# Kernel optimization log

Hardware: AMD Instinct MI355X
Metric: run time of the kernel (lower is better)

## Reference

```python
import jax, jax.numpy as jnp
import numpy as np

EMBED_DIM = 1024
NUM_HEADS = 16
HEAD_DIM = EMBED_DIM // NUM_HEADS


def setup_inputs() -> dict:
    key = jax.random.key(0)
    k_x, k_wqkv, k_bqkv, k_wout, k_bout = jax.random.split(key, 5)
    s = 1.0 / np.sqrt(EMBED_DIM)
    return {
        "x": jax.random.normal(k_x, (2, 2048, EMBED_DIM), dtype=jnp.float32),
        "w_qkv": jax.random.uniform(k_wqkv, (EMBED_DIM, 3 * EMBED_DIM), jnp.float32, -s, s),
        "b_qkv": jax.random.uniform(k_bqkv, (3 * EMBED_DIM,), jnp.float32, -s, s),
        "w_out": jax.random.uniform(k_wout, (EMBED_DIM, EMBED_DIM), jnp.float32, -s, s),
        "b_out": jax.random.uniform(k_bout, (EMBED_DIM,), jnp.float32, -s, s),
    }


def reference(x, w_qkv, b_qkv, w_out, b_out):
    B, S, D = x.shape
    H, Hd = NUM_HEADS, HEAD_DIM
    # qkv projection, then per-head chunk: layout matches torch view(B,S,H,3*Hd).chunk(3,-1)
    qkv = (x @ w_qkv + b_qkv).reshape(B, S, H, 3, Hd)  # [B,S,H,3,Hd]
    q = qkv[..., 0, :]  # [B,S,H,Hd]
    k = qkv[..., 1, :]
    v = qkv[..., 2, :]
    scale = 1.0 / np.sqrt(Hd).astype(np.float32)
    scores = jnp.einsum("bqhd,bkhd->bhqk", q, k) * scale  # [B,H,S,S]
    probs = jax.nn.softmax(scores, axis=-1)
    out = jnp.einsum("bhqk,bkhd->bqhd", probs, v).reshape(B, S, D)
    return out @ w_out + b_out
```

## Files before the change

kernel.cpp:

```cpp
#include <hip/hip_runtime.h>
#include <hip/hip_bf16.h>


typedef __bf16 bf16;
typedef __bf16 bf16x8 __attribute__((ext_vector_type(8)));
typedef float  f32x4  __attribute__((ext_vector_type(4)));
typedef float  f32x16 __attribute__((ext_vector_type(16)));
typedef unsigned int uint;
typedef unsigned int uint2v __attribute__((ext_vector_type(2)));

__device__ __forceinline__ void gload_lds16(const void* g, void* l) {
  __builtin_amdgcn_global_load_lds(
      (const __attribute__((address_space(1))) unsigned int*)g,
      (__attribute__((address_space(3))) unsigned int*)l, 16, 0, 0);
}

__device__ __forceinline__ uint pkbf16(float lo, float hi) {
  union { bf16 h[2]; uint u; } t;
  t.h[0] = (bf16)lo; t.h[1] = (bf16)hi;
  return t.u;
}

__device__ __forceinline__ void pl32swapu(uint& a, uint& b) {
  uint2v r = __builtin_amdgcn_permlane32_swap(a, b, false, false);
  a = r.x; b = r.y;
}
__device__ __forceinline__ void pl32swapf(float& a, float& b) {
  uint ua = __builtin_bit_cast(uint, a), ub = __builtin_bit_cast(uint, b);
  pl32swapu(ua, ub);
  a = __builtin_bit_cast(float, ua); b = __builtin_bit_cast(float, ub);
}

__global__ __launch_bounds__(256) void k_convert(const float* __restrict__ in,
                                                 bf16* __restrict__ out, int n) {
  int i = (blockIdx.x * blockDim.x + threadIdx.x) * 8;
  if (i >= n) return;
  float4 a = *(const float4*)(in + i);
  float4 b = *(const float4*)(in + i + 4);
  bf16x8 o;
  o[0] = (bf16)a.x; o[1] = (bf16)a.y; o[2] = (bf16)a.z; o[3] = (bf16)a.w;
  o[4] = (bf16)b.x; o[5] = (bf16)b.y; o[6] = (bf16)b.z; o[7] = (bf16)b.w;
  *(bf16x8*)(out + i) = o;
}

template<bool PERM>
__global__ __launch_bounds__(256) void k_transpose(const float* __restrict__ in,
                                                   bf16* __restrict__ out, int K, int N) {
  __shared__ float tile[32][33];
  int n0 = blockIdx.x * 32, k0 = blockIdx.y * 32;
  int tx = threadIdx.x, ty = threadIdx.y;
#pragma unroll
  for (int i = 0; i < 4; i++)
    tile[ty + i * 8][tx] = in[(size_t)(k0 + ty + i * 8) * N + n0 + tx];
  __syncthreads();
#pragma unroll
  for (int i = 0; i < 4; i++) {
    int n = n0 + ty + i * 8;
    int row = n;
    if (PERM) {
      int rem = n % 192;
      row = (rem >> 6) * 1024 + (n / 192) * 64 + (rem & 63);
    }
    out[(size_t)row * K + k0 + tx] = (bf16)tile[tx][ty + i * 8];
  }
}

template<int BM, int BN>
__device__ __forceinline__ void gemm_tile(const bf16* __restrict__ A, const bf16* __restrict__ B,
                                          int K, int m0, int n0,
                                          bf16* As, bf16* Bs, f32x4 acc[BM / 32][BN / 32]) {
  const int tid  = threadIdx.x;
  const int lane = tid & 63;
  const int wr   = (tid >> 7) & 1;
  const int wc   = (tid >> 6) & 1;
  constexpr int LA = BM / 64, LB = BN / 64;
  auto stage = [&](int k0, int b) {
#pragma unroll
    for (int i = 0; i < LA; i++) {
      int row = i * 64 + (tid >> 2);
      int sw  = (tid & 3) ^ (row & 3);
      gload_lds16(A + (size_t)(m0 + row) * K + k0 + sw * 8, (char*)As + b * (BM * 64) + i * 4096 + tid * 16);
    }
#pragma unroll
    for (int i = 0; i < LB; i++) {
      int row = i * 64 + (tid >> 2);
      int sw  = (tid & 3) ^ (row & 3);
      gload_lds16(B + (size_t)(n0 + row) * K + k0 + sw * 8, (char*)Bs + b * (BN * 64) + i * 4096 + tid * 16);
    }
  };
  const int nk = K / 32;
  stage(0, 0); stage(32, 1); stage(64, 2);
  for (int t = 0; t < nk; t++) {
    if (t < nk - 2) {
      if constexpr (LA + LB == 4) asm volatile("s_waitcnt vmcnt(8)" ::: "memory");
      else                        asm volatile("s_waitcnt vmcnt(6)" ::: "memory");
    } else if (t < nk - 1) {
      if constexpr (LA + LB == 4) asm volatile("s_waitcnt vmcnt(4)" ::: "memory");
      else                        asm volatile("s_waitcnt vmcnt(3)" ::: "memory");
    } else {
      asm volatile("s_waitcnt vmcnt(0)" ::: "memory");
    }
    __builtin_amdgcn_s_barrier();
    asm volatile("" ::: "memory");
    if (t + 3 < nk) stage((t + 3) * 32, (t + 3) & 3);
    const int cur = t & 3;
    bf16x8 af[BM / 32], bfr[BN / 32];
#pragma unroll
    for (int r = 0; r < BM / 32; r++) {
      int ra = wr * (BM / 2) + r * 16 + (lane & 15);
      af[r]  = *(const bf16x8*)((const char*)As + cur * (BM * 64) + ra * 64 + ((((lane >> 4) << 4)) ^ ((ra & 3) << 4)));
    }
#pragma unroll
    for (int c = 0; c < BN / 32; c++) {
      int rb = wc * (BN / 2) + c * 16 + (lane & 15);
      bfr[c] = *(const bf16x8*)((const char*)Bs + cur * (BN * 64) + rb * 64 + ((((lane >> 4) << 4)) ^ ((rb & 3) << 4)));
    }
#pragma unroll
    for (int r = 0; r < BM / 32; r++)
#pragma unroll
      for (int c = 0; c < BN / 32; c++)
        acc[r][c] = __builtin_amdgcn_mfma_f32_16x16x32_bf16(af[r], bfr[c], acc[r][c], 0, 0, 0);
    asm volatile("" ::: "memory");
  }
}

__global__ __launch_bounds__(512, 2) void k_gemm_qkv(const bf16* __restrict__ A, const bf16* __restrict__ Bt,
                                                     const float* __restrict__ bias,
                                                     bf16* __restrict__ qb, bf16* __restrict__ kb,
                                                     bf16* __restrict__ vtb) {
  __shared__ char GS[131072];
  const int tid  = threadIdx.x;
  const int lane = tid & 63;
  const int wave = tid >> 6;
  const int wr   = wave >> 2;
  const int wc   = wave & 3;
  const int m0 = blockIdx.x * 256, n0 = blockIdx.y * 256;
  const int K = 1024;

  f32x4 acc[8][4];
  f32x4 zero = {0.f, 0.f, 0.f, 0.f};
#pragma unroll
  for (int ms = 0; ms < 8; ms++)
#pragma unroll
    for (int ns = 0; ns < 4; ns++) acc[ms][ns] = zero;

  auto stage = [&](int t, int b) {
    int k0 = t * 64;
#pragma unroll
    for (int i = 0; i < 4; i++) {
      int cid = i * 512 + tid;
      int row = cid >> 3, c = cid & 7;
      gload_lds16(A + (size_t)(m0 + row) * K + k0 + ((c ^ (row & 7)) * 8),
                  GS + b * 32768 + cid * 16);
    }
#pragma unroll
    for (int i = 0; i < 4; i++) {
      int cid = i * 512 + tid;
      int row = cid >> 3, c = cid & 7;
      gload_lds16(Bt + (size_t)(n0 + row) * K + k0 + ((c ^ (row & 7)) * 8),
                  GS + 65536 + b * 32768 + cid * 16);
    }
  };

  stage(0, 0);
  for (int t = 0; t < 16; t++) {
    const int b = t & 1;
    if (t + 1 < 16) {
      stage(t + 1, b ^ 1);
      asm volatile("s_waitcnt vmcnt(8)" ::: "memory");
    } else {
      asm volatile("s_waitcnt vmcnt(0)" ::: "memory");
    }
    __builtin_amdgcn_s_barrier();
    asm volatile("" ::: "memory");
    const char* Ab = GS + b * 32768;
    const char* Bb = GS + 65536 + b * 32768;
#pragma unroll
    for (int ks = 0; ks < 2; ks++) {
      bf16x8 af[8], bf_[4];
#pragma unroll
      for (int ms = 0; ms < 8; ms++) {
        int row = wr * 128 + ms * 16 + (lane & 15);
        int ch = (ks * 4 + (lane >> 4)) ^ (row & 7);
        af[ms] = *(const bf16x8*)(Ab + row * 128 + ch * 16);
      }
#pragma unroll
      for (int ns = 0; ns < 4; ns++) {
        int row = wc * 64 + ns * 16 + (lane & 15);
        int ch = (ks * 4 + (lane >> 4)) ^ (row & 7);
        bf_[ns] = *(const bf16x8*)(Bb + row * 128 + ch * 16);
      }
      __builtin_amdgcn_s_setprio(1);
#pragma unroll
      for (int ms = 0; ms < 8; ms++)
#pragma unroll
        for (int ns = 0; ns < 4; ns++)
          acc[ms][ns] = __builtin_amdgcn_mfma_f32_16x16x32_bf16(af[ms], bf_[ns], acc[ms][ns], 0, 0, 0);
      __builtin_amdgcn_s_setprio(0);
    }
    asm volatile("" ::: "memory");
    __builtin_amdgcn_s_barrier();
    asm volatile("" ::: "memory");
  }

  const int group = n0 >> 10;
  const int hb = (n0 & 1023) >> 6;
  const int b_ = m0 >> 11;
  const float QSs = 0.125f * 1.4426950408889634f;
  char* TL = GS;

  if (group < 2) {
#pragma unroll
    for (int ms = 0; ms < 8; ms++) {
      int mloc = wr * 128 + ms * 16 + ((lane >> 4) << 2);
#pragma unroll
      for (int ns = 0; ns < 4; ns++) {
        int nloc = wc * 64 + ns * 16 + (lane & 15);
        int np = n0 + nloc;
        float bv = bias[((np & 1023) >> 6) * 192 + group * 64 + (np & 63)];
#pragma unroll
        for (int g = 0; g < 4; g++) {
          float v = acc[ms][ns][g] + bv;
          if (group == 0) v *= QSs;
          int m = mloc + g;
          int byte = m * 512 + ((((nloc >> 3) ^ (m & 7)) << 4) | ((nloc & 7) << 1));
          *(bf16*)(TL + byte) = (bf16)v;
        }
      }
    }
    __syncthreads();
    bf16* dst = (group == 0) ? qb : kb;
#pragma unroll
    for (int it = 0; it < 16; it++) {
      int cid = it * 512 + tid;
      int row = cid >> 5, cc = cid & 31;
      int hh = hb + (cc >> 3), ck = cc & 7;
      bf16x8 v8 = *(const bf16x8*)(TL + row * 512 + ((cc ^ (row & 7)) << 4));
      *(bf16x8*)(dst + ((size_t)(b_ * 16 + hh) * 2048 + (m0 & 2047) + row) * 64 + ck * 8) = v8;
    }
  } else {
#pragma unroll
    for (int ms = 0; ms < 8; ms++) {
      int mloc = wr * 128 + ms * 16 + ((lane >> 4) << 2);
#pragma unroll
      for (int ns = 0; ns < 4; ns++) {
        int nloc = wc * 64 + ns * 16 + (lane & 15);
        int np = n0 + nloc;
        float bv = bias[((np & 1023) >> 6) * 192 + 2 * 64 + (np & 63)];
#pragma unroll
        for (int g = 0; g < 4; g++) {
          float v = acc[ms][ns][g] + bv;
          int m = mloc + g;
          int byte = nloc * 512 + ((((m >> 3) ^ (nloc & 7)) << 4) | ((m & 7) << 1));
          *(bf16*)(TL + byte) = (bf16)v;
        }
      }
    }
    __syncthreads();
#pragma unroll
    for (int it = 0; it < 16; it++) {
      int cid = it * 512 + tid;
      int row = cid >> 5, mc = cid & 31;
      int hh = hb + (row >> 6), dd = row & 63;
      bf16x8 v8 = *(const bf16x8*)(TL + row * 512 + ((mc ^ (row & 7)) << 4));
      *(bf16x8*)(vtb + ((size_t)(b_ * 16 + hh) * 64 + dd) * 2048 + (m0 & 2047) + mc * 8) = v8;
    }
  }
}

__global__ __launch_bounds__(256) void k_gemm_out(const bf16* __restrict__ A, const bf16* __restrict__ Bt,
                                                  const float* __restrict__ bias,
                                                  float* __restrict__ out) {
  __shared__ bf16 As[4 * 64 * 32];
  __shared__ bf16 Bs[4 * 128 * 32];
  int m0 = blockIdx.x * 64, n0 = blockIdx.y * 128;
  f32x4 zero = {0.f, 0.f, 0.f, 0.f};
  f32x4 acc[2][4];
#pragma unroll
  for (int r = 0; r < 2; r++)
#pragma unroll
    for (int c = 0; c < 4; c++) acc[r][c] = zero;
  gemm_tile<64, 128>(A, Bt, 1024, m0, n0, As, Bs, acc);
  const int lane = threadIdx.x & 63;
  const int wr = (threadIdx.x >> 7) & 1, wc = (threadIdx.x >> 6) & 1;
#pragma unroll
  for (int r = 0; r < 2; r++) {
    int mbase = m0 + wr * 32 + r * 16 + ((lane >> 4) << 2);
#pragma unroll
    for (int c = 0; c < 4; c++) {
      int n = n0 + wc * 64 + c * 16 + (lane & 15);
      float bv = bias[n];
#pragma unroll
      for (int g = 0; g < 4; g++)
        out[(size_t)(mbase + g) * 1024 + n] = acc[r][c][g] + bv;
    }
  }
}

__global__ __launch_bounds__(512, 4) void k_attn(const bf16* __restrict__ qb, const bf16* __restrict__ kb,
                                                 const bf16* __restrict__ vtb, bf16* __restrict__ ob) {
  __shared__ char SMEM[73728];
  const int tid  = threadIdx.x;
  const int lane = tid & 63;
  const int wave = tid >> 6;
  const int qsub = wave & 3;
  const int half = wave >> 2;
  const int ln31 = lane & 31;
  const int g    = lane >> 5;

  int l = blockIdx.x;
  int x = l & 7, j = l >> 3;
  int qt = j & 15;
  int bh = x * 4 + (j >> 4);

  const int q0 = qt * 128 + qsub * 32;

  bf16x8 qf[4];
  {
    const bf16* qp = qb + ((size_t)bh * 2048 + q0 + ln31) * 64 + g * 8;
#pragma unroll
    for (int dc = 0; dc < 4; dc++) qf[dc] = *(const bf16x8*)(qp + dc * 16);
  }

  const f32x16 z16 = 0.f;
  f32x16 O0 = 0.f, O1 = 0.f;
  float lacc[4] = {0.f, 0.f, 0.f, 0.f};

  const int rbo = ln31 * 144 + (g << 4);
  const char* kbs0 = SMEM + half * 9216 + rbo;
  const char* kbs1 = SMEM + 36864 + half * 9216 + rbo;
  const char* vbs0 = SMEM + 18432 + half * 9216 + rbo;
  const char* vbs1 = SMEM + 36864 + 18432 + half * 9216 + rbo;

  const int c1 = tid, r1 = c1 / 9, cc1 = c1 % 9;
  const int of1 = (cc1 == 8 ? 0 : cc1) * 8;
  const bf16* kg0a = kb  + ((size_t)bh * 2048 +        r1) * 64 + of1;
  const bf16* kg1a = kb  + ((size_t)bh * 2048 + 1024 + r1) * 64 + of1;
  const bf16* vg0a = vtb + ((size_t)bh * 64 + r1) * 2048 +        of1;
  const bf16* vg1a = vtb + ((size_t)bh * 64 + r1) * 2048 + 1024 + of1;
  const int se = tid >> 6;
  const int ce = 512 + (tid & 63), re = ce / 9, cce = ce % 9;
  const int ofe = (cce == 8 ? 0 : cce) * 8;
  const bf16* gext =
      (se == 0) ? kb  + ((size_t)bh * 2048 +        re) * 64 + ofe :
      (se == 1) ? kb  + ((size_t)bh * 2048 + 1024 + re) * 64 + ofe :
      (se == 2) ? vtb + ((size_t)bh * 64 + re) * 2048 +        ofe :
                  vtb + ((size_t)bh * 64 + re) * 2048 + 1024 + ofe;
  const size_t gadv = (se < 2) ? 4096 : 64;
  const int eoff = se * 9216 + ce * 16;

  auto stage = [&](int t, int s) {
    char* bs = SMEM + s * 36864;
    gload_lds16(kg0a + (size_t)t * 4096, bs +         c1 * 16);
    gload_lds16(kg1a + (size_t)t * 4096, bs + 9216  + c1 * 16);
    gload_lds16(vg0a + t * 64,           bs + 18432 + c1 * 16);
    gload_lds16(vg1a + t * 64,           bs + 27648 + c1 * 16);
    if (tid < 256) gload_lds16(gext + (size_t)t * gadv, bs + eoff);
  };

  auto smx = [&](f32x16& sv, bf16x8& f0, bf16x8& f1) {
#pragma unroll
    for (int r = 0; r < 16; r++) sv[r] = __builtin_amdgcn_exp2f(sv[r]);
#pragma unroll
    for (int r = 0; r < 4; r++)
      lacc[r] += (sv[r] + sv[r + 4]) + (sv[r + 8] + sv[r + 12]);
    uint a0 = pkbf16(sv[0], sv[1]), a1 = pkbf16(sv[2], sv[3]);
    uint a2 = pkbf16(sv[4], sv[5]), a3 = pkbf16(sv[6], sv[7]);
    pl32swapu(a0, a2); pl32swapu(a1, a3);
    union { uint w[4]; bf16x8 v; } pa;
    pa.w[0] = a0; pa.w[1] = a1; pa.w[2] = a2; pa.w[3] = a3;
    f0 = pa.v;
    uint b0 = pkbf16(sv[8], sv[9]),  b1 = pkbf16(sv[10], sv[11]);
    uint b2 = pkbf16(sv[12], sv[13]), b3 = pkbf16(sv[14], sv[15]);
    pl32swapu(b0, b2); pl32swapu(b1, b3);
    union { uint w[4]; bf16x8 v; } pb;
    pb.w[0] = b0; pb.w[1] = b1; pb.w[2] = b2; pb.w[3] = b3;
    f1 = pb.v;
  };

  stage(0, 0);
  for (int t = 0; t < 16; t++) {
    asm volatile("s_waitcnt vmcnt(0)" ::: "memory");
    __builtin_amdgcn_s_barrier();
    asm volatile("" ::: "memory");
    if (t + 1 < 16) stage(t + 1, (t + 1) & 1);

    const char* Kb = (t & 1) ? kbs1 : kbs0;
    const char* Vb = (t & 1) ? vbs1 : vbs0;

    f32x16 sA, sB;
    __builtin_amdgcn_s_setprio(1);
    sA = __builtin_amdgcn_mfma_f32_32x32x16_bf16(*(const bf16x8*)(Kb +    0), qf[0], z16, 0, 0, 0);
    sB = __builtin_amdgcn_mfma_f32_32x32x16_bf16(*(const bf16x8*)(Kb + 4608), qf[0], z16, 0, 0, 0);
#pragma unroll
    for (int dc = 1; dc < 4; dc++) {
      sA = __builtin_amdgcn_mfma_f32_32x32x16_bf16(*(const bf16x8*)(Kb + dc * 32),        qf[dc], sA, 0, 0, 0);
      sB = __builtin_amdgcn_mfma_f32_32x32x16_bf16(*(const bf16x8*)(Kb + 4608 + dc * 32), qf[dc], sB, 0, 0, 0);
    }
    __builtin_amdgcn_s_setprio(0);

    bf16x8 fA0, fA1, fB0, fB1;
    smx(sA, fA0, fA1);
    __builtin_amdgcn_s_setprio(1);
    O0 = __builtin_amdgcn_mfma_f32_32x32x16_bf16(*(const bf16x8*)(Vb +    0), fA0, O0, 0, 0, 0);
    O1 = __builtin_amdgcn_mfma_f32_32x32x16_bf16(*(const bf16x8*)(Vb + 4608), fA0, O1, 0, 0, 0);
    O0 = __builtin_amdgcn_mfma_f32_32x32x16_bf16(*(const bf16x8*)(Vb +   32), fA1, O0, 0, 0, 0);
    O1 = __builtin_amdgcn_mfma_f32_32x32x16_bf16(*(const bf16x8*)(Vb + 4640), fA1, O1, 0, 0, 0);
    __builtin_amdgcn_s_setprio(0);
    smx(sB, fB0, fB1);
    __builtin_amdgcn_s_setprio(1);
    O0 = __builtin_amdgcn_mfma_f32_32x32x16_bf16(*(const bf16x8*)(Vb +   64), fB0, O0, 0, 0, 0);
    O1 = __builtin_amdgcn_mfma_f32_32x32x16_bf16(*(const bf16x8*)(Vb + 4672), fB0, O1, 0, 0, 0);
    O0 = __builtin_amdgcn_mfma_f32_32x32x16_bf16(*(const bf16x8*)(Vb +   96), fB1, O0, 0, 0, 0);
    O1 = __builtin_amdgcn_mfma_f32_32x32x16_bf16(*(const bf16x8*)(Vb + 4704), fB1, O1, 0, 0, 0);
    __builtin_amdgcn_s_setprio(0);
    asm volatile("" ::: "memory");
  }

  float l_r = (lacc[0] + lacc[1]) + (lacc[2] + lacc[3]);
  { float o = l_r; pl32swapf(l_r, o); l_r += o; }

  float* Opart = (float*)SMEM;
  float* Ls    = (float*)(SMEM + 36864);
  __syncthreads();
  if (half == 1) {
    float* my = Opart + (qsub * 64 + lane) * 36;
#pragma unroll
    for (int c = 0; c < 4; c++) {
      f32x4 a = {O0[c * 4], O0[c * 4 + 1], O0[c * 4 + 2], O0[c * 4 + 3]};
      f32x4 b = {O1[c * 4], O1[c * 4 + 1], O1[c * 4 + 2], O1[c * 4 + 3]};
      *(f32x4*)(my + c * 4) = a;
      *(f32x4*)(my + 16 + c * 4) = b;
    }
    if (lane < 32) Ls[qsub * 32 + ln31] = l_r;
  }
  __syncthreads();
  bf16 (*Os)[32][72] = reinterpret_cast<bf16 (*)[32][72]>(SMEM + 40960);
  if (half == 0) {
    const float* pr = Opart + (qsub * 64 + lane) * 36;
#pragma unroll
    for (int c = 0; c < 4; c++) {
      f32x4 a = *(const f32x4*)(pr + c * 4);
      f32x4 b = *(const f32x4*)(pr + 16 + c * 4);
#pragma unroll
      for (int k = 0; k < 4; k++) { O0[c * 4 + k] += a[k]; O1[c * 4 + k] += b[k]; }
    }
    l_r += Ls[qsub * 32 + ln31];
    float inv = 1.0f / l_r;
#pragma unroll
    for (int r = 0; r < 16; r++) {
      int d0 = (r & 3) + 8 * (r >> 2) + 4 * g;
      Os[qsub][ln31][d0]      = (bf16)(O0[r] * inv);
      Os[qsub][ln31][d0 + 32] = (bf16)(O1[r] * inv);
    }
  }
  __syncthreads();
  if (half == 0) {
    int b_ = bh >> 4, h = bh & 15;
#pragma unroll
    for (int it = 0; it < 4; it++) {
      int cid = it * 64 + lane;
      int row = cid >> 3, c = cid & 7;
      bf16x8 v8o = *(const bf16x8*)&Os[qsub][row][c * 8];
      *(bf16x8*)(ob + ((size_t)(b_ * 2048 + q0 + row)) * 1024 + h * 64 + c * 8) = v8o;
    }
  }
}

extern "C" void kernel_launch(void* const* d_in, const int* in_sizes, int n_in,
                              void* d_out, int out_size, void* d_ws, size_t ws_size,
                              hipStream_t stream) {
  const float* x     = (const float*)d_in[0];
  const float* w_qkv = (const float*)d_in[1];
  const float* b_qkv = (const float*)d_in[2];
  const float* w_out = (const float*)d_in[3];
  const float* b_out = (const float*)d_in[4];
  float* out = (float*)d_out;

  char* ws = (char*)d_ws;
  bf16* xb  = (bf16*)ws;
  bf16* wqT = (bf16*)(ws + (8ull  << 20));
  bf16* woT = (bf16*)(ws + (14ull << 20));
  bf16* qb  = (bf16*)(ws + (16ull << 20));
  bf16* kb  = (bf16*)(ws + (24ull << 20));
  bf16* vtb = (bf16*)(ws + (32ull << 20));

  k_convert<<<2048, 256, 0, stream>>>(x, xb, 4194304);
  k_transpose<true><<<dim3(96, 32), dim3(32, 8), 0, stream>>>(w_qkv, wqT, 1024, 3072);
  k_transpose<false><<<dim3(32, 32), dim3(32, 8), 0, stream>>>(w_out, woT, 1024, 1024);
  k_gemm_qkv<<<dim3(16, 12), 512, 0, stream>>>(xb, wqT, b_qkv, qb, kb, vtb);
  k_attn<<<512, 512, 0, stream>>>(qb, kb, vtb, xb);
  k_gemm_out<<<dim3(64, 8), 256, 0, stream>>>(xb, woT, b_out, out);
}
```

Before: 116.6 us.

## Software-pipeline attention loop: split K/V staging and overlap QK with PV

Splits tile staging into separate K and V loads and restructures the main loop so that the PV product for tile t runs while the QK product and softmax for tile t+1 are computed, with two tiles of prefetch in flight. The goal is to hide global-to-LDS load latency and the softmax VALU work behind MFMA work by staggering stages across iterations. It adds an extra barrier per iteration and relies on correct double-buffer reuse timing, which carries a risk of races if the wait and barrier placement is wrong.

Result: no change. 116.3 us (-0.2%).

```diff
diff --git a/kernel.cpp b/kernel.cpp
--- a/kernel.cpp
+++ b/kernel.cpp
@@ -349,14 +349,20 @@
   const size_t gadv = (se < 2) ? 4096 : 64;
   const int eoff = se * 9216 + ce * 16;
 
-  auto stage = [&](int t, int s) {
+  auto stageK = [&](int t, int s) {
     char* bs = SMEM + s * 36864;
-    gload_lds16(kg0a + (size_t)t * 4096, bs +         c1 * 16);
-    gload_lds16(kg1a + (size_t)t * 4096, bs + 9216  + c1 * 16);
-    gload_lds16(vg0a + t * 64,           bs + 18432 + c1 * 16);
-    gload_lds16(vg1a + t * 64,           bs + 27648 + c1 * 16);
-    if (tid < 256) gload_lds16(gext + (size_t)t * gadv, bs + eoff);
-  };
+    gload_lds16(kg0a + (size_t)t * 4096, bs +        c1 * 16);
+    gload_lds16(kg1a + (size_t)t * 4096, bs + 9216 + c1 * 16);
+    if (tid < 256 && se < 2) gload_lds16(gext + (size_t)t * gadv, bs + eoff);
+  };
+  auto stageV = [&](int t, int s) {
+    char* bs = SMEM + s * 36864;
+    gload_lds16(vg0a + t * 64, bs + 18432 + c1 * 16);
+    gload_lds16(vg1a + t * 64, bs + 27648 + c1 * 16);
+    if (tid < 256 && se >= 2) gload_lds16(gext + (size_t)t * gadv, bs + eoff);
+  };
+
+  bf16x8 fA0, fA1, fB0, fB1;
 
   auto smx = [&](f32x16& sv, bf16x8& f0, bf16x8& f1) {
 #pragma unroll
@@ -378,18 +384,7 @@
     f1 = pb.v;
   };
 
-  stage(0, 0);
-  for (int t = 0; t < 16; t++) {
-    asm volatile("s_waitcnt vmcnt(0)" ::: "memory");
-    __builtin_amdgcn_s_barrier();
-    asm volatile("" ::: "memory");
-    if (t + 1 < 16) stage(t + 1, (t + 1) & 1);
-
-    const char* Kb = (t & 1) ? kbs1 : kbs0;
-    const char* Vb = (t & 1) ? vbs1 : vbs0;
-
-    f32x16 sA, sB;
-    __builtin_amdgcn_s_setprio(1);
+  auto qk = [&](const char* Kb, f32x16& sA, f32x16& sB) {
     sA = __builtin_amdgcn_mfma_f32_32x32x16_bf16(*(const bf16x8*)(Kb +    0), qf[0], z16, 0, 0, 0);
     sB = __builtin_amdgcn_mfma_f32_32x32x16_bf16(*(const bf16x8*)(Kb + 4608), qf[0], z16, 0, 0, 0);
 #pragma unroll
@@ -397,25 +392,58 @@
       sA = __builtin_amdgcn_mfma_f32_32x32x16_bf16(*(const bf16x8*)(Kb + dc * 32),        qf[dc], sA, 0, 0, 0);
       sB = __builtin_amdgcn_mfma_f32_32x32x16_bf16(*(const bf16x8*)(Kb + 4608 + dc * 32), qf[dc], sB, 0, 0, 0);
     }
-    __builtin_amdgcn_s_setprio(0);
-
-    bf16x8 fA0, fA1, fB0, fB1;
-    smx(sA, fA0, fA1);
-    __builtin_amdgcn_s_setprio(1);
+  };
+
+  auto pv = [&](const char* Vb) {
     O0 = __builtin_amdgcn_mfma_f32_32x32x16_bf16(*(const bf16x8*)(Vb +    0), fA0, O0, 0, 0, 0);
     O1 = __builtin_amdgcn_mfma_f32_32x32x16_bf16(*(const bf16x8*)(Vb + 4608), fA0, O1, 0, 0, 0);
     O0 = __builtin_amdgcn_mfma_f32_32x32x16_bf16(*(const bf16x8*)(Vb +   32), fA1, O0, 0, 0, 0);
     O1 = __builtin_amdgcn_mfma_f32_32x32x16_bf16(*(const bf16x8*)(Vb + 4640), fA1, O1, 0, 0, 0);
-    __builtin_amdgcn_s_setprio(0);
-    smx(sB, fB0, fB1);
-    __builtin_amdgcn_s_setprio(1);
     O0 = __builtin_amdgcn_mfma_f32_32x32x16_bf16(*(const bf16x8*)(Vb +   64), fB0, O0, 0, 0, 0);
     O1 = __builtin_amdgcn_mfma_f32_32x32x16_bf16(*(const bf16x8*)(Vb + 4672), fB0, O1, 0, 0, 0);
     O0 = __builtin_amdgcn_mfma_f32_32x32x16_bf16(*(const bf16x8*)(Vb +   96), fB1, O0, 0, 0, 0);
     O1 = __builtin_amdgcn_mfma_f32_32x32x16_bf16(*(const bf16x8*)(Vb + 4704), fB1, O1, 0, 0, 0);
+  };
+
+  stageK(0, 0); stageV(0, 0);
+  stageK(1, 1); stageV(1, 1);
+  asm volatile("s_waitcnt vmcnt(0)" ::: "memory");
+  __builtin_amdgcn_s_barrier();
+  asm volatile("" ::: "memory");
+  {
+    f32x16 sA, sB;
+    __builtin_amdgcn_s_setprio(1);
+    qk(kbs0, sA, sB);
     __builtin_amdgcn_s_setprio(0);
-    asm volatile("" ::: "memory");
-  }
+    smx(sA, fA0, fA1);
+    smx(sB, fB0, fB1);
+  }
+
+  for (int t = 0; t < 15; t++) {
+    asm volatile("" ::: "memory");
+    __builtin_amdgcn_s_barrier();
+    asm volatile("" ::: "memory");
+    if (t + 2 < 16) stageK(t + 2, t & 1);
+    const char* Vb = (t & 1) ? vbs1 : vbs0;
+    __builtin_amdgcn_s_setprio(1);
+    pv(Vb);
+    __builtin_amdgcn_s_setprio(0);
+    asm volatile("" ::: "memory");
+    __builtin_amdgcn_s_barrier();
+    asm volatile("" ::: "memory");
+    if (t + 2 < 16) stageV(t + 2, t & 1);
+    const char* Kb = (t & 1) ? kbs0 : kbs1;
+    f32x16 sA, sB;
+    __builtin_amdgcn_s_setprio(1);
+    qk(Kb, sA, sB);
+    __builtin_amdgcn_s_setprio(0);
+    smx(sA, fA0, fA1);
+    smx(sB, fB0, fB1);
+    asm volatile("s_waitcnt vmcnt(0)" ::: "memory");
+  }
+  __builtin_amdgcn_s_barrier();
+  asm volatile("" ::: "memory");
+  pv(vbs1);
 
   float l_r = (lacc[0] + lacc[1]) + (lacc[2] + lacc[3]);
   { float o = l_r; pl32swapf(l_r, o); l_r += o; }
```

## Interleave QKV GEMM loads and MFMA in quarter-tile phases with finer barriers

Applied to the files above, without the earlier changes.

Rewrites the main loop of the QKV projection GEMM into a ping-pong schedule. Each K-tile is split into four sub-tile phases (A/B halves), and each phase's LDS reads, global-to-LDS prefetch and MFMA block are separated by barriers so memory traffic overlaps with compute at a finer grain. Global and LDS addresses are precomputed per thread to reduce address arithmetic. The cost is more barriers and a fragile vmcnt accounting that must match the issue order exactly.

After: 112.4 us. -3.6%, faster.

```diff
diff --git a/kernel.cpp b/kernel.cpp
--- a/kernel.cpp
+++ b/kernel.cpp
@@ -74,18 +74,18 @@
   const int wr   = (tid >> 7) & 1;
   const int wc   = (tid >> 6) & 1;
   constexpr int LA = BM / 64, LB = BN / 64;
-  auto stage = [&](int k0, int b) {
+  auto stage = [&](int k0v, int b) {
 #pragma unroll
     for (int i = 0; i < LA; i++) {
       int row = i * 64 + (tid >> 2);
       int sw  = (tid & 3) ^ (row & 3);
-      gload_lds16(A + (size_t)(m0 + row) * K + k0 + sw * 8, (char*)As + b * (BM * 64) + i * 4096 + tid * 16);
+      gload_lds16(A + (size_t)(m0 + row) * K + k0v + sw * 8, (char*)As + b * (BM * 64) + i * 4096 + tid * 16);
     }
 #pragma unroll
     for (int i = 0; i < LB; i++) {
       int row = i * 64 + (tid >> 2);
       int sw  = (tid & 3) ^ (row & 3);
-      gload_lds16(B + (size_t)(n0 + row) * K + k0 + sw * 8, (char*)Bs + b * (BN * 64) + i * 4096 + tid * 16);
+      gload_lds16(B + (size_t)(n0 + row) * K + k0v + sw * 8, (char*)Bs + b * (BN * 64) + i * 4096 + tid * 16);
     }
   };
   const int nk = K / 32;
@@ -144,64 +144,141 @@
 #pragma unroll
     for (int ns = 0; ns < 4; ns++) acc[ms][ns] = zero;
 
-  auto stage = [&](int t, int b) {
-    int k0 = t * 64;
-#pragma unroll
-    for (int i = 0; i < 4; i++) {
-      int cid = i * 512 + tid;
-      int row = cid >> 3, c = cid & 7;
-      gload_lds16(A + (size_t)(m0 + row) * K + k0 + ((c ^ (row & 7)) * 8),
-                  GS + b * 32768 + cid * 16);
-    }
-#pragma unroll
-    for (int i = 0; i < 4; i++) {
-      int cid = i * 512 + tid;
-      int row = cid >> 3, c = cid & 7;
-      gload_lds16(Bt + (size_t)(n0 + row) * K + k0 + ((c ^ (row & 7)) * 8),
-                  GS + 65536 + b * 32768 + cid * 16);
-    }
-  };
-
-  stage(0, 0);
-  for (int t = 0; t < 16; t++) {
-    const int b = t & 1;
-    if (t + 1 < 16) {
-      stage(t + 1, b ^ 1);
-      asm volatile("s_waitcnt vmcnt(8)" ::: "memory");
+  const int ccs = tid & 7;
+  int rA[2], rB[2];
+  {
+    int lr0 = tid >> 3;
+    rA[0] = lr0;
+    rB[0] = (lr0 & 31) + ((lr0 >> 5) << 6);
+    int lr1 = 64 + lr0;
+    rA[1] = (lr1 & 63) + 128;
+    rB[1] = (lr1 & 31) + ((lr1 >> 5) << 6);
+  }
+  const bf16* Agp[2]; const bf16* Bgp[2];
+  int Alo[2], Blo[2];
+#pragma unroll
+  for (int j = 0; j < 2; j++) {
+    Agp[j] = A  + (size_t)(m0 + rA[j]) * K + (ccs ^ (rA[j] & 7)) * 8;
+    Alo[j] = rA[j] * 128 + ccs * 16;
+    Bgp[j] = Bt + (size_t)(n0 + rB[j]) * K + (ccs ^ (rB[j] & 7)) * 8;
+    Blo[j] = rB[j] * 128 + ccs * 16;
+  }
+  auto stA = [&](int t, int h) {
+    int b = t & 1;
+#pragma unroll
+    for (int j = 0; j < 2; j++)
+      gload_lds16(Agp[j] + (size_t)(h * 64) * K + t * 64, GS + b * 32768 + Alo[j] + h * 8192);
+  };
+  auto stB = [&](int t, int h) {
+    int b = t & 1;
+#pragma unroll
+    for (int j = 0; j < 2; j++)
+      gload_lds16(Bgp[j] + (size_t)(h * 32) * K + t * 64, GS + 65536 + b * 32768 + Blo[j] + h * 4096);
+  };
+
+  bf16x8 af[4][2], bf0[2][2], bf1[2][2];
+  auto rdA = [&](const char* Ab, int mh) {
+#pragma unroll
+    for (int ms = 0; ms < 4; ms++)
+#pragma unroll
+      for (int ks = 0; ks < 2; ks++) {
+        int row = wr * 128 + (mh * 4 + ms) * 16 + (lane & 15);
+        int ch = (ks * 4 + (lane >> 4)) ^ (row & 7);
+        af[ms][ks] = *(const bf16x8*)(Ab + row * 128 + ch * 16);
+      }
+  };
+  auto rdB = [&](const char* Bb, int nh, bf16x8 (&bfx)[2][2]) {
+#pragma unroll
+    for (int ns = 0; ns < 2; ns++)
+#pragma unroll
+      for (int ks = 0; ks < 2; ks++) {
+        int row = wc * 64 + (nh * 2 + ns) * 16 + (lane & 15);
+        int ch = (ks * 4 + (lane >> 4)) ^ (row & 7);
+        bfx[ns][ks] = *(const bf16x8*)(Bb + row * 128 + ch * 16);
+      }
+  };
+  auto mm = [&](int mh, int nh, bf16x8 (&bfx)[2][2]) {
+    __builtin_amdgcn_s_setprio(1);
+#pragma unroll
+    for (int ks = 0; ks < 2; ks++)
+#pragma unroll
+      for (int ms = 0; ms < 4; ms++)
+#pragma unroll
+        for (int ns = 0; ns < 2; ns++)
+          acc[mh * 4 + ms][nh * 2 + ns] =
+              __builtin_amdgcn_mfma_f32_16x16x32_bf16(af[ms][ks], bfx[ns][ks],
+                                                      acc[mh * 4 + ms][nh * 2 + ns], 0, 0, 0);
+    __builtin_amdgcn_s_setprio(0);
+  };
+
+#define BARRIER do { asm volatile("" ::: "memory"); __builtin_amdgcn_s_barrier(); \
+                     asm volatile("" ::: "memory"); } while (0)
+
+  stA(0, 0); stB(0, 0); stB(0, 1); stA(0, 1);
+  stA(1, 0); stB(1, 0); stB(1, 1);
+  asm volatile("s_waitcnt vmcnt(6)" ::: "memory");
+  __builtin_amdgcn_s_barrier();
+  asm volatile("" ::: "memory");
+
+  for (int I = 0; I < 8; I++) {
+    const int T = 2 * I;
+    const char* Ab0 = GS;
+    const char* Bb0 = GS + 65536;
+    const char* Ab1 = GS + 32768;
+    const char* Bb1 = GS + 65536 + 32768;
+    const bool m2 = (T + 2 < 16), m3 = (T + 3 < 16);
+
+    rdA(Ab0, 0); rdB(Bb0, 0, bf0);
+    stA(T + 1, 1);
+    BARRIER;
+    mm(0, 0, bf0);
+
+    rdB(Bb0, 1, bf1);
+    if (m2) stA(T + 2, 0);
+    BARRIER;
+    mm(0, 1, bf1);
+
+    rdA(Ab0, 1);
+    if (m2) stB(T + 2, 0);
+    BARRIER;
+    mm(1, 0, bf0);
+
+    if (m2) {
+      stB(T + 2, 1);
+      asm volatile("s_waitcnt vmcnt(6)" ::: "memory");
     } else {
       asm volatile("s_waitcnt vmcnt(0)" ::: "memory");
     }
     __builtin_amdgcn_s_barrier();
     asm volatile("" ::: "memory");
-    const char* Ab = GS + b * 32768;
-    const char* Bb = GS + 65536 + b * 32768;
-#pragma unroll
-    for (int ks = 0; ks < 2; ks++) {
-      bf16x8 af[8], bf_[4];
-#pragma unroll
-      for (int ms = 0; ms < 8; ms++) {
-        int row = wr * 128 + ms * 16 + (lane & 15);
-        int ch = (ks * 4 + (lane >> 4)) ^ (row & 7);
-        af[ms] = *(const bf16x8*)(Ab + row * 128 + ch * 16);
-      }
-#pragma unroll
-      for (int ns = 0; ns < 4; ns++) {
-        int row = wc * 64 + ns * 16 + (lane & 15);
-        int ch = (ks * 4 + (lane >> 4)) ^ (row & 7);
-        bf_[ns] = *(const bf16x8*)(Bb + row * 128 + ch * 16);
-      }
-      __builtin_amdgcn_s_setprio(1);
-#pragma unroll
-      for (int ms = 0; ms < 8; ms++)
-#pragma unroll
-        for (int ns = 0; ns < 4; ns++)
-          acc[ms][ns] = __builtin_amdgcn_mfma_f32_16x16x32_bf16(af[ms], bf_[ns], acc[ms][ns], 0, 0, 0);
-      __builtin_amdgcn_s_setprio(0);
-    }
-    asm volatile("" ::: "memory");
+    mm(1, 1, bf1);
+
+    rdA(Ab1, 0); rdB(Bb1, 0, bf0);
+    if (m2) stA(T + 2, 1);
+    BARRIER;
+    mm(0, 0, bf0);
+
+    rdB(Bb1, 1, bf1);
+    if (m3) stA(T + 3, 0);
+    BARRIER;
+    mm(0, 1, bf1);
+
+    rdA(Ab1, 1);
+    if (m3) stB(T + 3, 0);
+    BARRIER;
+    mm(1, 0, bf0);
+
+    if (m3) {
+      stB(T + 3, 1);
+      asm volatile("s_waitcnt vmcnt(6)" ::: "memory");
+    } else {
+      asm volatile("s_waitcnt vmcnt(0)" ::: "memory");
+    }
     __builtin_amdgcn_s_barrier();
     asm volatile("" ::: "memory");
-  }
+    mm(1, 1, bf1);
+  }
+#undef BARRIER
 
   const int group = n0 >> 10;
   const int hb = (n0 & 1023) >> 6;
```
